# Optimization experiments

Hardware: AMD Instinct MI355X
Metric: run time of the kernel (lower is better)

The kernel has to match this reference:

```python
import jax, jax.numpy as jnp
import numpy as np

B, S, D = 2, 4096, 512
H, DK, DV = 8, 64, 64
LN_EPS = 1e-5
ATTN_EPS = 1e-6


def layer_norm(x, g, b):
    mu = jnp.mean(x, axis=-1, keepdims=True)
    var = jnp.var(x, axis=-1, keepdims=True)
    return (x - mu) * jax.lax.rsqrt(var + LN_EPS) * g + b


def setup_inputs() -> dict:
    key = jax.random.key(0)
    ks = jax.random.split(key, 12)
    s = 1.0 / np.sqrt(D)
    inp = {
        "Q": jax.random.normal(ks[0], (B, S, D), jnp.float32),
        "K": jax.random.normal(ks[1], (B, S, D), jnp.float32),
        "V": jax.random.normal(ks[2], (B, S, D), jnp.float32),
        "W_q": jax.random.normal(ks[3], (D, H * DK), jnp.float32) * s,
        "W_k": jax.random.normal(ks[4], (D, H * DK), jnp.float32) * s,
        "W_v": jax.random.normal(ks[5], (D, H * DV), jnp.float32) * s,
        "W_o": jax.random.normal(ks[6], (H * DV, D), jnp.float32) * s,
        "ln1_g": jnp.ones((D,), jnp.float32),
        "ln1_b": jnp.zeros((D,), jnp.float32),
        "ln2_g": jnp.ones((D,), jnp.float32),
        "ln2_b": jnp.zeros((D,), jnp.float32),
        "w1": jax.random.normal(ks[7], (4 * D, D), jnp.float32) * s,  # torch Linear: (out, in)
        "b1": jnp.zeros((4 * D,), jnp.float32),
        "w2": jax.random.normal(ks[8], (D, 4 * D), jnp.float32) * (1.0 / np.sqrt(4 * D)),
        "b2": jnp.zeros((D,), jnp.float32),
    }
    return inp


def reference(Q, K, V, W_q, W_k, W_v, W_o, ln1_g, ln1_b, ln2_g, ln2_b, w1, b1, w2, b2):
    Qn = layer_norm(Q, ln1_g, ln1_b)
    # project and split heads: [B,S,H,dk] -> [B,H,S,dk]
    q = (Qn @ W_q).reshape(B, S, H, DK).transpose(0, 2, 1, 3)
    k = (K @ W_k).reshape(B, S, H, DK).transpose(0, 2, 1, 3)
    v = (V @ W_v).reshape(B, S, H, DV).transpose(0, 2, 1, 3)
    scores = jnp.einsum("bhqd,bhkd->bhqk", q, k) / (np.sqrt(DK) + ATTN_EPS)
    attn = jax.nn.softmax(scores, axis=-1)  # same as max-subtract softmax
    ctx = jnp.einsum("bhqk,bhkd->bhqd", attn, v)
    ctx = ctx.transpose(0, 2, 1, 3).reshape(B, S, H * DV)
    att_out = ctx @ W_o  # dropout = identity (eval)
    X = Q + att_out
    Xn = layer_norm(X, ln2_g, ln2_b)
    h = jax.nn.gelu(Xn @ w1.T + b1, approximate=False)
    ffn = h @ w2.T + b2
    return X + ffn
```

## Files before the change

### kernel.cpp

```cpp
#include <hip/hip_runtime.h>

typedef unsigned short u16;
typedef __attribute__((ext_vector_type(8))) short short8;
typedef __attribute__((ext_vector_type(4))) float f32x4;
typedef __attribute__((ext_vector_type(16))) float f32x16;
typedef __attribute__((ext_vector_type(4))) unsigned u32x4;

struct __align__(8) us4 { u16 x, y, z, w; };
struct __align__(8) ui2 { unsigned x, y; };

#define CEXP (1.44269504089f / (8.0f + 1e-6f))

__device__ __forceinline__ u16 f2bf(float f) {
  unsigned u = __builtin_bit_cast(unsigned, f);
  unsigned r = (u + 0x7FFFu + ((u >> 16) & 1u)) >> 16;
  return (u16)r;
}

__device__ __forceinline__ unsigned pack_bf2_trunc(float a, float b) {
  return __builtin_amdgcn_perm(__builtin_bit_cast(unsigned, b),
                               __builtin_bit_cast(unsigned, a), 0x07060302u);
}

__device__ __forceinline__ void async_load16(const void* g, void* l) {
  __builtin_amdgcn_global_load_lds((const __attribute__((address_space(1))) void*)g,
                                   (__attribute__((address_space(3))) void*)l, 16, 0, 0);
}

__global__ void prep_weights(const float* __restrict__ Wq, const float* __restrict__ Wk,
                             const float* __restrict__ Wv, const float* __restrict__ Wo,
                             const float* __restrict__ w1, const float* __restrict__ w2,
                             u16* __restrict__ wqkvT, u16* __restrict__ woT,
                             u16* __restrict__ w1b, u16* __restrict__ w2b) {
  const int z = blockIdx.y;
  const int stride = gridDim.x * blockDim.x;
  const int i0 = blockIdx.x * blockDim.x + threadIdx.x;
  if (z < 4) {
    const float* src = z == 0 ? Wq : z == 1 ? Wk : z == 2 ? Wv : Wo;
    u16* dst = z < 3 ? wqkvT + z * 512 * 512 : woT;
    const float scale = (z == 0) ? CEXP : 1.0f;
    for (int i = i0; i < 512 * 512; i += stride) {
      int n = i >> 9, k = i & 511;
      dst[i] = f2bf(src[k * 512 + n] * scale);
    }
  } else {
    const float* src = z == 4 ? w1 : w2;
    u16* dst = z == 4 ? w1b : w2b;
    for (int i = i0; i < 2048 * 512; i += stride) dst[i] = f2bf(src[i]);
  }
}

template <bool KV>
__launch_bounds__(128)
__global__ void ln_cast(const float* __restrict__ X, const float* __restrict__ gw,
                        const float* __restrict__ bw, u16* __restrict__ Y,
                        const float* __restrict__ Kin, const float* __restrict__ Vin,
                        u16* __restrict__ Kb, u16* __restrict__ Vb) {
  const int row = blockIdx.x, t = threadIdx.x;
  const size_t base = (size_t)row * 512;
  float4 x = ((const float4*)(X + base))[t];
  float s = x.x + x.y + x.z + x.w;
  float ss = x.x * x.x + x.y * x.y + x.z * x.z + x.w * x.w;
#pragma unroll
  for (int off = 32; off > 0; off >>= 1) {
    s += __shfl_xor(s, off);
    ss += __shfl_xor(ss, off);
  }
  __shared__ float red[4];
  if ((t & 63) == 0) { red[(t >> 6) * 2] = s; red[(t >> 6) * 2 + 1] = ss; }
  __syncthreads();
  const float tot = red[0] + red[2], tss = red[1] + red[3];
  const float mu = tot * (1.0f / 512.0f);
  const float var = tss * (1.0f / 512.0f) - mu * mu;
  const float rs = rsqrtf(var + 1e-5f);
  float4 g4 = ((const float4*)gw)[t];
  float4 b4 = ((const float4*)bw)[t];
  us4 o;
  o.x = f2bf((x.x - mu) * rs * g4.x + b4.x);
  o.y = f2bf((x.y - mu) * rs * g4.y + b4.y);
  o.z = f2bf((x.z - mu) * rs * g4.z + b4.z);
  o.w = f2bf((x.w - mu) * rs * g4.w + b4.w);
  ((us4*)(Y + base))[t] = o;
  if constexpr (KV) {
    float4 k4 = ((const float4*)(Kin + base))[t];
    float4 v4 = ((const float4*)(Vin + base))[t];
    us4 ko, vo;
    ko.x = f2bf(k4.x); ko.y = f2bf(k4.y); ko.z = f2bf(k4.z); ko.w = f2bf(k4.w);
    vo.x = f2bf(v4.x); vo.y = f2bf(v4.y); vo.z = f2bf(v4.z); vo.w = f2bf(v4.w);
    ((us4*)(Kb + base))[t] = ko;
    ((us4*)(Vb + base))[t] = vo;
  }
}

__launch_bounds__(256, 3)
__global__ void gemm_qkv(const u16* __restrict__ Aq, const u16* __restrict__ Ak,
                         const u16* __restrict__ Av, const u16* __restrict__ Bt,
                         u16* __restrict__ qb, u16* __restrict__ kb, u16* __restrict__ vtb) {
  __shared__ __align__(16) u16 sA[128 * 32];
  __shared__ __align__(16) u16 sB[128 * 32];
  const int tid = threadIdx.x;
  const int wave = tid >> 6, lane = tid & 63;
  const int l15 = lane & 15, quad = lane >> 4;
  const int qsw = (quad ^ ((l15 >> 1) & 3)) * 8;
  const int m0 = blockIdx.x * 128, n0 = blockIdx.y * 128;
  const int sel = n0 >> 9;
  const u16* A = sel == 0 ? Aq : sel == 1 ? Ak : Av;
  const int wm = (wave >> 1) * 64, wn = (wave & 1) * 64;
  const int u0 = wave * 64 + lane, u1 = u0 + 256;
  const int sw0 = ((u0 & 3) ^ ((u0 >> 3) & 3)) * 8;
  const int K = 512;

  const u16* a0 = A + (size_t)(m0 + (u0 >> 2)) * K + sw0;
  const u16* a1 = A + (size_t)(m0 + (u1 >> 2)) * K + sw0;
  const u16* b0 = Bt + (size_t)(n0 + (u0 >> 2)) * K + sw0;
  const u16* b1p = Bt + (size_t)(n0 + (u1 >> 2)) * K + sw0;

  f32x4 acc[4][4] = {};
  for (int k0 = 0; k0 < K; k0 += 32) {
    async_load16(a0 + k0, &sA[wave * 512]);
    async_load16(a1 + k0, &sA[2048 + wave * 512]);
    async_load16(b0 + k0, &sB[wave * 512]);
    async_load16(b1p + k0, &sB[2048 + wave * 512]);
    __syncthreads();
    short8 af[4], bfr[4];
#pragma unroll
    for (int i = 0; i < 4; i++)
      af[i] = *(const short8*)&sA[(wm + i * 16 + l15) * 32 + qsw];
#pragma unroll
    for (int j = 0; j < 4; j++)
      bfr[j] = *(const short8*)&sB[(wn + j * 16 + l15) * 32 + qsw];
#pragma unroll
    for (int i = 0; i < 4; i++)
#pragma unroll
      for (int j = 0; j < 4; j++)
        acc[i][j] = __builtin_amdgcn_mfma_f32_16x16x32_bf16(af[i], bfr[j], acc[i][j], 0, 0, 0);
    __syncthreads();
  }

#pragma unroll
  for (int i = 0; i < 4; i++) {
#pragma unroll
    for (int j = 0; j < 4; j++) {
      const int ocol = ((n0 + wn) & 511) + j * 16 + l15;
      const int row0 = m0 + wm + i * 16 + quad * 4;
      if (sel < 2) {
        u16* C = sel == 0 ? qb : kb;
#pragma unroll
        for (int r = 0; r < 4; r++) C[(size_t)(row0 + r) * 512 + ocol] = f2bf(acc[i][j][r]);
      } else {
        const int b = row0 >> 12, s0 = row0 & 4095;
        const int hh = ocol >> 6, cc = ocol & 63;
        us4 pk;
        pk.x = f2bf(acc[i][j][0]); pk.y = f2bf(acc[i][j][1]);
        pk.z = f2bf(acc[i][j][2]); pk.w = f2bf(acc[i][j][3]);
        *(us4*)&vtb[((size_t)((b * 8 + hh) * 64 + cc) << 12) + s0] = pk;
      }
    }
  }
}

template <int EP, int TN, int LB>
__launch_bounds__(256, LB)
__global__ void gemm_bt(const u16* __restrict__ A, const u16* __restrict__ Bt,
                        int M, int N, int K, void* __restrict__ Cp,
                        const float* __restrict__ bias, const float* __restrict__ res) {
  constexpr int MI = (TN == 128) ? 4 : 2;
  __shared__ __align__(16) u16 sA[128 * 32];
  __shared__ __align__(16) u16 sB[TN * 32];
  const int tid = threadIdx.x;
  const int wave = tid >> 6, lane = tid & 63;
  const int l15 = lane & 15, quad = lane >> 4;
  const int qsw = (quad ^ ((l15 >> 1) & 3)) * 8;
  const int m0 = blockIdx.x * 128, n0 = blockIdx.y * TN;
  const int wm = (TN == 128) ? (wave >> 1) * 64 : wave * 32;
  const int wn = (TN == 128) ? (wave & 1) * 64 : 0;
  const int u0 = wave * 64 + lane, u1 = u0 + 256;
  const int sw0 = ((u0 & 3) ^ ((u0 >> 3) & 3)) * 8;

  const u16* a0 = A + (size_t)(m0 + (u0 >> 2)) * K + sw0;
  const u16* a1 = A + (size_t)(m0 + (u1 >> 2)) * K + sw0;
  const u16* b0 = Bt + (size_t)(n0 + (u0 >> 2)) * K + sw0;

  f32x4 acc[MI][4] = {};
  for (int k0 = 0; k0 < K; k0 += 32) {
    async_load16(a0 + k0, &sA[wave * 512]);
    async_load16(a1 + k0, &sA[2048 + wave * 512]);
    async_load16(b0 + k0, &sB[wave * 512]);
    if constexpr (TN == 128) {
      const u16* b1p = Bt + (size_t)(n0 + (u1 >> 2)) * K + sw0;
      async_load16(b1p + k0, &sB[2048 + wave * 512]);
    }
    __syncthreads();
    short8 af[MI], bfr[4];
#pragma unroll
    for (int i = 0; i < MI; i++)
      af[i] = *(const short8*)&sA[(wm + i * 16 + l15) * 32 + qsw];
#pragma unroll
    for (int j = 0; j < 4; j++)
      bfr[j] = *(const short8*)&sB[(wn + j * 16 + l15) * 32 + qsw];
#pragma unroll
    for (int i = 0; i < MI; i++)
#pragma unroll
      for (int j = 0; j < 4; j++)
        acc[i][j] = __builtin_amdgcn_mfma_f32_16x16x32_bf16(af[i], bfr[j], acc[i][j], 0, 0, 0);
    __syncthreads();
  }

#pragma unroll
  for (int i = 0; i < MI; i++) {
#pragma unroll
    for (int j = 0; j < 4; j++) {
      const int col = n0 + wn + j * 16 + l15;
      const int row0 = m0 + wm + i * 16 + quad * 4;
      if (EP == 2) {
        float* C = (float*)Cp;
#pragma unroll
        for (int r = 0; r < 4; r++) {
          size_t idx = (size_t)(row0 + r) * N + col;
          C[idx] = acc[i][j][r] + res[idx];
        }
      } else if (EP == 3) {
        u16* C = (u16*)Cp;
        const float bv = bias[col];
#pragma unroll
        for (int r = 0; r < 4; r++) {
          float xx = acc[i][j][r] + bv;
          float gl = 0.5f * xx * (1.0f + erff(xx * 0.70710678118f));
          C[(size_t)(row0 + r) * N + col] = f2bf(gl);
        }
      } else {
        float* C = (float*)Cp;
        const float bv = bias[col];
#pragma unroll
        for (int r = 0; r < 4; r++) {
          size_t idx = (size_t)(row0 + r) * N + col;
          C[idx] = acc[i][j][r] + bv + res[idx];
        }
      }
    }
  }
}

__launch_bounds__(512, 2)
__global__ void attn_kernel(const u16* __restrict__ qb, const u16* __restrict__ kb,
                            const u16* __restrict__ vtb, u16* __restrict__ ctx) {
  __shared__ __align__(16) u16 smem[24576];
  const int tid = threadIdx.x;
  const int wave = tid >> 6, lane = tid & 63;
  const int l31 = lane & 31, hi = lane >> 5;
  const int qg = wave >> 1, kh = wave & 1;
  const int bh = blockIdx.x, b = bh >> 3, h = bh & 7;
  const int q0 = blockIdx.y * 128;
  const size_t rb = (size_t)b * 4096;
  const int qrow = q0 + qg * 32 + l31;

  short8 qf[4];
#pragma unroll
  for (int ks = 0; ks < 4; ks++)
    qf[ks] = *(const short8*)&qb[(rb + qrow) * 512 + h * 64 + ks * 16 + hi * 8];

  const int srow = tid >> 3, ssl = (tid & 7) ^ (srow & 7);
  const u16* kp = kb + (rb + srow) * 512 + h * 64 + ssl * 8;
  const u16* vp = vtb + (size_t)(bh * 64 + srow) * 4096 + ssl * 8;

#define STAGE(bi)                                  \
  {                                                \
    async_load16(kp, &smem[(bi) * 4096 + tid * 8]);\
    async_load16(vp, &smem[12288 + (bi) * 4096 + tid * 8]); \
    kp += 64 * 512; vp += 64;                      \
  }

  f32x16 ov[2] = {};
  float l_part = 0.f;

  STAGE(0);
  STAGE(1);
  asm volatile("s_waitcnt vmcnt(2)" ::: "memory");
  __syncthreads();

  int cur = 0, nxt = 2;
  for (int t = 0; t < 64; t++) {
    if (t < 62) {
      STAGE(nxt);
      nxt = nxt == 2 ? 0 : nxt + 1;
    }
    const u16* K_ = smem + cur * 4096;
    const u16* V_ = smem + 12288 + cur * 4096;
    cur = cur == 2 ? 0 : cur + 1;
    f32x16 st = {};
    __builtin_amdgcn_s_setprio(1);
#pragma unroll
    for (int ks = 0; ks < 4; ks++) {
      const int row = kh * 32 + l31;
      const int sl = (ks * 2 + hi) ^ (row & 7);
      short8 kf = *(const short8*)&K_[row * 64 + sl * 8];
      st = __builtin_amdgcn_mfma_f32_32x32x16_bf16(kf, qf[ks], st, 0, 0, 0);
    }
    __builtin_amdgcn_s_setprio(0);
    float p[16];
#pragma unroll
    for (int i = 0; i < 16; i++) p[i] = __builtin_amdgcn_exp2f(st[i]);
#pragma unroll
    for (int i = 0; i < 16; i += 4)
      l_part += (p[i] + p[i + 1]) + (p[i + 2] + p[i + 3]);
    unsigned x0 = pack_bf2_trunc(p[0], p[1]), x1 = pack_bf2_trunc(p[2], p[3]);
    unsigned x2 = pack_bf2_trunc(p[4], p[5]), x3 = pack_bf2_trunc(p[6], p[7]);
    unsigned x4 = pack_bf2_trunc(p[8], p[9]), x5 = pack_bf2_trunc(p[10], p[11]);
    unsigned x6 = pack_bf2_trunc(p[12], p[13]), x7 = pack_bf2_trunc(p[14], p[15]);
    auto r0 = __builtin_amdgcn_permlane32_swap(x0, x2, false, false);
    auto r1 = __builtin_amdgcn_permlane32_swap(x1, x3, false, false);
    auto r2 = __builtin_amdgcn_permlane32_swap(x4, x6, false, false);
    auto r3 = __builtin_amdgcn_permlane32_swap(x5, x7, false, false);
    u32x4 w0 = {r0[0], r1[0], r0[1], r1[1]};
    u32x4 w1 = {r2[0], r3[0], r2[1], r3[1]};
    short8 pf0 = __builtin_bit_cast(short8, w0);
    short8 pf1 = __builtin_bit_cast(short8, w1);
    __builtin_amdgcn_s_setprio(1);
#pragma unroll
    for (int vb = 0; vb < 2; vb++) {
      const int row = vb * 32 + l31;
      const int sl0 = (kh * 4 + hi) ^ (row & 7);
      const int sl1 = (kh * 4 + 2 + hi) ^ (row & 7);
      short8 vf0 = *(const short8*)&V_[row * 64 + sl0 * 8];
      short8 vf1 = *(const short8*)&V_[row * 64 + sl1 * 8];
      ov[vb] = __builtin_amdgcn_mfma_f32_32x32x16_bf16(vf0, pf0, ov[vb], 0, 0, 0);
      ov[vb] = __builtin_amdgcn_mfma_f32_32x32x16_bf16(vf1, pf1, ov[vb], 0, 0, 0);
    }
    __builtin_amdgcn_s_setprio(0);
    if (t < 63) {
      if (t < 62)
        asm volatile("s_waitcnt vmcnt(2)" ::: "memory");
      else
        asm volatile("s_waitcnt vmcnt(0)" ::: "memory");
      __syncthreads();
    }
  }
#undef STAGE

  float l2 = l_part + __shfl_xor(l_part, 32);
  __syncthreads();
  float* mrg = (float*)smem;
  float* mrgl = (float*)smem + 8192;
  if (kh == 1) {
#pragma unroll
    for (int vb = 0; vb < 2; vb++)
#pragma unroll
      for (int e = 0; e < 16; e++)
        mrg[(qg * 32 + vb * 16 + e) * 64 + lane] = ov[vb][e];
    mrgl[qg * 64 + lane] = l2;
  }
  __syncthreads();
  if (kh == 0) {
    const float inv = 1.0f / (l2 + mrgl[qg * 64 + lane]);
#pragma unroll
    for (int vb = 0; vb < 2; vb++) {
#pragma unroll
      for (int rg = 0; rg < 4; rg++) {
        us4 o;
        o.x = f2bf((ov[vb][rg * 4 + 0] + mrg[(qg * 32 + vb * 16 + rg * 4 + 0) * 64 + lane]) * inv);
        o.y = f2bf((ov[vb][rg * 4 + 1] + mrg[(qg * 32 + vb * 16 + rg * 4 + 1) * 64 + lane]) * inv);
        o.z = f2bf((ov[vb][rg * 4 + 2] + mrg[(qg * 32 + vb * 16 + rg * 4 + 2) * 64 + lane]) * inv);
        o.w = f2bf((ov[vb][rg * 4 + 3] + mrg[(qg * 32 + vb * 16 + rg * 4 + 3) * 64 + lane]) * inv);
        *(us4*)&ctx[(rb + qrow) * 512 + h * 64 + vb * 32 + rg * 8 + hi * 4] = o;
      }
    }
  }
}

extern "C" void kernel_launch(void* const* d_in, const int* in_sizes, int n_in,
                              void* d_out, int out_size, void* d_ws, size_t ws_size,
                              hipStream_t stream) {
  (void)in_sizes; (void)n_in; (void)out_size; (void)ws_size;
  const float* Q = (const float*)d_in[0];
  const float* K = (const float*)d_in[1];
  const float* V = (const float*)d_in[2];
  const float* W_q = (const float*)d_in[3];
  const float* W_k = (const float*)d_in[4];
  const float* W_v = (const float*)d_in[5];
  const float* W_o = (const float*)d_in[6];
  const float* ln1_g = (const float*)d_in[7];
  const float* ln1_b = (const float*)d_in[8];
  const float* ln2_g = (const float*)d_in[9];
  const float* ln2_b = (const float*)d_in[10];
  const float* w1 = (const float*)d_in[11];
  const float* b1 = (const float*)d_in[12];
  const float* w2 = (const float*)d_in[13];
  const float* b2 = (const float*)d_in[14];

  char* w = (char*)d_ws;
  const size_t MB = 1u << 20;
  u16* wqkvT = (u16*)(w);
  u16* woT = (u16*)(w + 3 * MB / 2);
  u16* w1b = (u16*)(w + 2 * MB);
  u16* w2b = (u16*)(w + 4 * MB);
  u16* Qn  = (u16*)(w + 6 * MB);
  u16* Kb  = (u16*)(w + 14 * MB);
  u16* Vb  = (u16*)(w + 22 * MB);
  u16* qb  = (u16*)(w + 30 * MB);
  u16* kb  = (u16*)(w + 38 * MB);
  u16* vtb = (u16*)(w + 46 * MB);
  u16* ctx = (u16*)(w + 54 * MB);
  float* X = (float*)(w + 62 * MB);
  u16* Xn  = (u16*)(w + 6 * MB);
  u16* hb  = (u16*)(w + 14 * MB);

  prep_weights<<<dim3(128, 6), 256, 0, stream>>>(W_q, W_k, W_v, W_o, w1, w2,
                                                 wqkvT, woT, w1b, w2b);
  ln_cast<true><<<8192, 128, 0, stream>>>(Q, ln1_g, ln1_b, Qn, K, V, Kb, Vb);
  gemm_qkv<<<dim3(64, 12), 256, 0, stream>>>(Qn, Kb, Vb, wqkvT, qb, kb, vtb);
  attn_kernel<<<dim3(16, 32), 512, 0, stream>>>(qb, kb, vtb, ctx);
  gemm_bt<2, 64, 3><<<dim3(64, 8), 256, 0, stream>>>(ctx, woT, 8192, 512, 512, X, nullptr, Q);
  ln_cast<false><<<8192, 128, 0, stream>>>(X, ln2_g, ln2_b, Xn, nullptr, nullptr, nullptr, nullptr);
  gemm_bt<3, 128, 3><<<dim3(64, 16), 256, 0, stream>>>(Xn, w1b, 8192, 2048, 512, hb, b1, nullptr);
  gemm_bt<4, 64, 3><<<dim3(64, 8), 256, 0, stream>>>(hb, w2b, 8192, 512, 2048, (float*)d_out, b2, X);
}
```

Baseline: 328.6 us.

## Store K in MFMA-fragment layout and load K directly to registers in attention

The K projection epilogue now writes K in a per-head, per-32-key fragment layout matching the MFMA operand order. The attention kernel then loads K fragments straight from global memory into registers, skipping the LDS staging. Only V stays in LDS, now double-buffered, which cuts shared memory use. The loop is unrolled by two with a prefetch of the next tile issued after the QK MFMAs. The trade-off is exposed global load latency for K with shallower prefetch depth and a full vmcnt(0) wait each iteration, plus scattered 2-byte stores in the K epilogue.

```diff
diff --git a/kernel.cpp b/kernel.cpp
--- a/kernel.cpp
+++ b/kernel.cpp
@@ -143,10 +143,21 @@
     for (int j = 0; j < 4; j++) {
       const int ocol = ((n0 + wn) & 511) + j * 16 + l15;
       const int row0 = m0 + wm + i * 16 + quad * 4;
-      if (sel < 2) {
-        u16* C = sel == 0 ? qb : kb;
-#pragma unroll
-        for (int r = 0; r < 4; r++) C[(size_t)(row0 + r) * 512 + ocol] = f2bf(acc[i][j][r]);
+      if (sel == 0) {
+#pragma unroll
+        for (int r = 0; r < 4; r++) qb[(size_t)(row0 + r) * 512 + ocol] = f2bf(acc[i][j][r]);
+      } else if (sel == 1) {
+        const int d = ocol & 63, hh2 = ocol >> 6;
+        const int ks = d >> 4, hik = (d >> 3) & 1, e = d & 7;
+#pragma unroll
+        for (int r = 0; r < 4; r++) {
+          const int row = row0 + r;
+          const int bb = row >> 12, keys = row & 4095;
+          const size_t addr =
+              (((size_t)((bb * 8 + hh2) * 128 + (keys >> 5)) * 4 + ks) * 64 +
+               (keys & 31) + 32 * hik) * 8 + e;
+          kb[addr] = f2bf(acc[i][j][r]);
+        }
       } else {
         const int b = row0 >> 12, s0 = row0 & 4095;
         const int hh = ocol >> 6, cc = ocol & 63;
@@ -242,9 +253,9 @@
 }
 
 __launch_bounds__(512, 2)
-__global__ void attn_kernel(const u16* __restrict__ qb, const u16* __restrict__ kb,
+__global__ void attn_kernel(const u16* __restrict__ qb, const u16* __restrict__ kfrag,
                             const u16* __restrict__ vtb, u16* __restrict__ ctx) {
-  __shared__ __align__(16) u16 smem[24576];
+  __shared__ __align__(16) u16 smem[16896];
   const int tid = threadIdx.x;
   const int wave = tid >> 6, lane = tid & 63;
   const int l31 = lane & 31, hi = lane >> 5;
@@ -259,83 +270,82 @@
   for (int ks = 0; ks < 4; ks++)
     qf[ks] = *(const short8*)&qb[(rb + qrow) * 512 + h * 64 + ks * 16 + hi * 8];
 
+  int voff[2][2];
+#pragma unroll
+  for (int vb = 0; vb < 2; vb++) {
+    const int vrow = vb * 32 + l31;
+    voff[vb][0] = vrow * 64 + (((kh * 4 + hi) ^ (vrow & 7))) * 8;
+    voff[vb][1] = vrow * 64 + (((kh * 4 + 2 + hi) ^ (vrow & 7))) * 8;
+  }
+
   const int srow = tid >> 3, ssl = (tid & 7) ^ (srow & 7);
-  const u16* kp = kb + (rb + srow) * 512 + h * 64 + ssl * 8;
   const u16* vp = vtb + (size_t)(bh * 64 + srow) * 4096 + ssl * 8;
-
-#define STAGE(bi)                                  \
-  {                                                \
-    async_load16(kp, &smem[(bi) * 4096 + tid * 8]);\
-    async_load16(vp, &smem[12288 + (bi) * 4096 + tid * 8]); \
-    kp += 64 * 512; vp += 64;                      \
-  }
-
+  const int sdst = tid * 8;
+
+  const u16* kp = kfrag + ((size_t)(bh * 128 + kh) * 4) * 512 + lane * 8;
+
+  short8 kc[4];
   f32x16 ov[2] = {};
   float l_part = 0.f;
 
-  STAGE(0);
-  STAGE(1);
-  asm volatile("s_waitcnt vmcnt(2)" ::: "memory");
+#pragma unroll
+  for (int ks = 0; ks < 4; ks++) kc[ks] = *(const short8*)(kp + ks * 512);
+  kp += 4096;
+  async_load16(vp, &smem[sdst]);
+  vp += 64;
+  asm volatile("s_waitcnt vmcnt(0)" ::: "memory");
   __syncthreads();
 
-  int cur = 0, nxt = 2;
-  for (int t = 0; t < 64; t++) {
-    if (t < 62) {
-      STAGE(nxt);
-      nxt = nxt == 2 ? 0 : nxt + 1;
-    }
-    const u16* K_ = smem + cur * 4096;
-    const u16* V_ = smem + 12288 + cur * 4096;
-    cur = cur == 2 ? 0 : cur + 1;
-    f32x16 st = {};
-    __builtin_amdgcn_s_setprio(1);
-#pragma unroll
-    for (int ks = 0; ks < 4; ks++) {
-      const int row = kh * 32 + l31;
-      const int sl = (ks * 2 + hi) ^ (row & 7);
-      short8 kf = *(const short8*)&K_[row * 64 + sl * 8];
-      st = __builtin_amdgcn_mfma_f32_32x32x16_bf16(kf, qf[ks], st, 0, 0, 0);
-    }
-    __builtin_amdgcn_s_setprio(0);
-    float p[16];
-#pragma unroll
-    for (int i = 0; i < 16; i++) p[i] = __builtin_amdgcn_exp2f(st[i]);
-#pragma unroll
-    for (int i = 0; i < 16; i += 4)
-      l_part += (p[i] + p[i + 1]) + (p[i + 2] + p[i + 3]);
-    unsigned x0 = pack_bf2_trunc(p[0], p[1]), x1 = pack_bf2_trunc(p[2], p[3]);
-    unsigned x2 = pack_bf2_trunc(p[4], p[5]), x3 = pack_bf2_trunc(p[6], p[7]);
-    unsigned x4 = pack_bf2_trunc(p[8], p[9]), x5 = pack_bf2_trunc(p[10], p[11]);
-    unsigned x6 = pack_bf2_trunc(p[12], p[13]), x7 = pack_bf2_trunc(p[14], p[15]);
-    auto r0 = __builtin_amdgcn_permlane32_swap(x0, x2, false, false);
-    auto r1 = __builtin_amdgcn_permlane32_swap(x1, x3, false, false);
-    auto r2 = __builtin_amdgcn_permlane32_swap(x4, x6, false, false);
-    auto r3 = __builtin_amdgcn_permlane32_swap(x5, x7, false, false);
-    u32x4 w0 = {r0[0], r1[0], r0[1], r1[1]};
-    u32x4 w1 = {r2[0], r3[0], r2[1], r3[1]};
-    short8 pf0 = __builtin_bit_cast(short8, w0);
-    short8 pf1 = __builtin_bit_cast(short8, w1);
-    __builtin_amdgcn_s_setprio(1);
-#pragma unroll
-    for (int vb = 0; vb < 2; vb++) {
-      const int row = vb * 32 + l31;
-      const int sl0 = (kh * 4 + hi) ^ (row & 7);
-      const int sl1 = (kh * 4 + 2 + hi) ^ (row & 7);
-      short8 vf0 = *(const short8*)&V_[row * 64 + sl0 * 8];
-      short8 vf1 = *(const short8*)&V_[row * 64 + sl1 * 8];
-      ov[vb] = __builtin_amdgcn_mfma_f32_32x32x16_bf16(vf0, pf0, ov[vb], 0, 0, 0);
-      ov[vb] = __builtin_amdgcn_mfma_f32_32x32x16_bf16(vf1, pf1, ov[vb], 0, 0, 0);
-    }
-    __builtin_amdgcn_s_setprio(0);
-    if (t < 63) {
-      if (t < 62)
-        asm volatile("s_waitcnt vmcnt(2)" ::: "memory");
-      else
-        asm volatile("s_waitcnt vmcnt(0)" ::: "memory");
-      __syncthreads();
-    }
-  }
-#undef STAGE
+#define BODY(VB, COND)                                                              \
+  {                                                                                 \
+    f32x16 st = {};                                                                 \
+    __builtin_amdgcn_s_setprio(1);                                                  \
+    _Pragma("unroll") for (int ks = 0; ks < 4; ks++)                                \
+      st = __builtin_amdgcn_mfma_f32_32x32x16_bf16(kc[ks], qf[ks], st, 0, 0, 0);    \
+    __builtin_amdgcn_s_setprio(0);                                                  \
+    if (COND) {                                                                     \
+      _Pragma("unroll") for (int ks = 0; ks < 4; ks++)                              \
+        kc[ks] = *(const short8*)(kp + ks * 512);                                   \
+      kp += 4096;                                                                   \
+      async_load16(vp, &smem[(1 - (VB)) * 4096 + sdst]);                            \
+      vp += 64;                                                                     \
+    }                                                                               \
+    float p[16];                                                                    \
+    _Pragma("unroll") for (int i = 0; i < 16; i++)                                  \
+        p[i] = __builtin_amdgcn_exp2f(st[i]);                                       \
+    _Pragma("unroll") for (int i = 0; i < 16; i += 4)                               \
+        l_part += (p[i] + p[i + 1]) + (p[i + 2] + p[i + 3]);                        \
+    unsigned x0 = pack_bf2_trunc(p[0], p[1]), x1 = pack_bf2_trunc(p[2], p[3]);      \
+    unsigned x2 = pack_bf2_trunc(p[4], p[5]), x3 = pack_bf2_trunc(p[6], p[7]);      \
+    unsigned x4 = pack_bf2_trunc(p[8], p[9]), x5 = pack_bf2_trunc(p[10], p[11]);    \
+    unsigned x6 = pack_bf2_trunc(p[12], p[13]), x7 = pack_bf2_trunc(p[14], p[15]);  \
+    auto r0 = __builtin_amdgcn_permlane32_swap(x0, x2, false, false);               \
+    auto r1 = __builtin_amdgcn_permlane32_swap(x1, x3, false, false);               \
+    auto r2 = __builtin_amdgcn_permlane32_swap(x4, x6, false, false);               \
+    auto r3 = __builtin_amdgcn_permlane32_swap(x5, x7, false, false);               \
+    u32x4 w0 = {r0[0], r1[0], r0[1], r1[1]};                                        \
+    u32x4 w1 = {r2[0], r3[0], r2[1], r3[1]};                                        \
+    short8 pf0 = __builtin_bit_cast(short8, w0);                                    \
+    short8 pf1 = __builtin_bit_cast(short8, w1);                                    \
+    __builtin_amdgcn_s_setprio(1);                                                  \
+    _Pragma("unroll") for (int vb = 0; vb < 2; vb++) {                              \
+      short8 vf0 = *(const short8*)&smem[(VB) * 4096 + voff[vb][0]];                \
+      short8 vf1 = *(const short8*)&smem[(VB) * 4096 + voff[vb][1]];                \
+      ov[vb] = __builtin_amdgcn_mfma_f32_32x32x16_bf16(vf0, pf0, ov[vb], 0, 0, 0);  \
+      ov[vb] = __builtin_amdgcn_mfma_f32_32x32x16_bf16(vf1, pf1, ov[vb], 0, 0, 0);  \
+    }                                                                               \
+    __builtin_amdgcn_s_setprio(0);                                                  \
+    if (COND) {                                                                     \
+      asm volatile("s_waitcnt vmcnt(0)" ::: "memory");                              \
+      __syncthreads();                                                              \
+    }                                                                               \
+  }
+
+  for (int g = 0; g < 32; g++) {
+    BODY(0, true);
+    BODY(1, (g < 31));
+  }
+#undef BODY
 
   float l2 = l_part + __shfl_xor(l_part, 32);
   __syncthreads();
```

Result: no change. 330.1 us (+0.4%).
